# Kernel tuning notes

Hardware: AMD Instinct MI355X
Metric: run time of the kernel (lower is better)

Reference implementation:

```python
import jax, jax.numpy as jnp
import numpy as np

N_NODES, N_EDGES, D, N_RELS = 50000, 600000, 128, 460


def setup_inputs() -> dict:
    key = jax.random.key(0)
    ks = jax.random.split(key, 8)
    h = jax.random.normal(ks[0], (N_NODES, D), dtype=jnp.float32)
    emb_rel = jax.random.normal(ks[1], (N_RELS, D), dtype=jnp.float32)
    attn_fc_w = jax.random.normal(ks[2], (D, 3 * D), dtype=jnp.float32) * 0.05   # Linear(3D->D), weight [out,in]
    attn_fc2_w = jax.random.normal(ks[3], (1, D), dtype=jnp.float32) * 0.05     # Linear(D->1)
    loop_weight = jax.random.normal(ks[4], (D, D), dtype=jnp.float32) * 0.05
    edge_src = jax.random.randint(ks[5], (N_EDGES,), 0, N_NODES)
    edge_dst = jax.random.randint(ks[6], (N_EDGES,), 0, N_NODES)
    edge_type = jax.random.randint(ks[7], (N_EDGES,), 0, N_RELS)
    return {"h": h, "emb_rel": emb_rel, "attn_fc_w": attn_fc_w,
            "attn_fc2_w": attn_fc2_w, "loop_weight": loop_weight,
            "edge_src": edge_src, "edge_dst": edge_dst, "edge_type": edge_type}


def reference(h, emb_rel, attn_fc_w, attn_fc2_w, loop_weight, edge_src, edge_dst, edge_type):
    n = h.shape[0]
    # --- per-edge gather ---
    hs = h[edge_src]            # [E, D] src features (mailbox 'e_h')
    ht = h[edge_dst]            # [E, D]
    rel = emb_rel[edge_type]    # [E, D]
    # --- concat-MLP attention: leaky_relu(fc2(fc1([hs|ht|rel]))) ---
    z2 = jnp.concatenate([hs, ht, rel], axis=1)          # [E, 3D]
    a = z2 @ attn_fc_w.T                                  # [E, D]
    e = jax.nn.leaky_relu(a @ attn_fc2_w.T)               # [E, 1], slope 0.01 (torch default)
    # --- per-destination segment softmax ---
    m = jax.ops.segment_max(e, edge_dst, num_segments=n)  # [N, 1]
    m = jnp.where(jnp.isfinite(m), m, jnp.float32(0.0))   # empty nodes -> -inf; neutralize
    ex = jnp.exp(e - m[edge_dst])                         # [E, 1]
    den = jax.ops.segment_sum(ex, edge_dst, num_segments=n)
    alpha = ex / den[edge_dst]                            # [E, 1]
    # --- weighted scatter-sum of src features ---
    node_repr = jax.ops.segment_sum(alpha * hs, edge_dst, num_segments=n)  # [N, D]
    # --- self-loop ---
    node_repr = node_repr + h @ loop_weight
    return node_repr
```

## Files before the change

kernel.cpp:

```cpp
#include <hip/hip_runtime.h>

#define N_NODES 50000
#define N_EDGES 600000
#define D 128
#define N_RELS 460
#define CAP_LOG 6

typedef unsigned short u16;
typedef __attribute__((ext_vector_type(8))) short bf16x8;
typedef __attribute__((ext_vector_type(4))) float f32x4;

enum : int {
    OFF_W      = 0,
    OFF_S1     = 384,
    OFF_S2     = 50384,
    OFF_S3     = 100384,
    OFF_COUNTS = 100864,
    OFF_CSR    = 900864,
    OFF_HB     = 4100864,
};

#define NODE_WAVES   12500
#define REL_WAVES    115
#define SCORE_BLOCKS 3154
#define GEMM_BLOCKS  782
#define ZERO_BLOCKS  196
#define FILL_BLOCKS  293
#define WT_STRIDE    136

__device__ __forceinline__ u16 f2bf(float f) {
    unsigned u = __float_as_uint(f);
    unsigned r = u + 0x7FFFu + ((u >> 16) & 1u);
    return (u16)(r >> 16);
}
__device__ __forceinline__ float blo(unsigned u) { return __uint_as_float(u << 16); }
__device__ __forceinline__ float bhi(unsigned u) { return __uint_as_float(u & 0xFFFF0000u); }

__global__ __launch_bounds__(256) void k_prep(
        const float* __restrict__ fc1, const float* __restrict__ fc2,
        const float* __restrict__ W, const float* __restrict__ h,
        float* __restrict__ w, int* __restrict__ counts,
        u16* __restrict__ hb, float* __restrict__ out) {
    __shared__ u16 Ws[D * WT_STRIDE];
    int t = threadIdx.x;
    if (blockIdx.x < GEMM_BLOCKS) {
        for (int i = t; i < (D * D) / 4; i += 256) {
            float4 v = ((const float4*)W)[i];
            int k  = i >> 5;
            int n0 = (i & 31) * 4;
            Ws[(n0 + 0) * WT_STRIDE + k] = f2bf(v.x);
            Ws[(n0 + 1) * WT_STRIDE + k] = f2bf(v.y);
            Ws[(n0 + 2) * WT_STRIDE + k] = f2bf(v.z);
            Ws[(n0 + 3) * WT_STRIDE + k] = f2bf(v.w);
        }
        __syncthreads();

        int wave = t >> 6, lane = t & 63;
        int quad = lane >> 4, m16 = lane & 15;
        int nbase = blockIdx.x * 64 + wave * 16;

        f32x4 acc[8];
        #pragma unroll
        for (int cg = 0; cg < 8; ++cg) acc[cg] = (f32x4){0.f, 0.f, 0.f, 0.f};

        int arow = nbase + m16;
        if (arow >= N_NODES) arow = N_NODES - 1;
        const float* aptr = h + (size_t)arow * D + quad * 8;
        u16* hbp = hb + (size_t)arow * D + quad * 8;

        #pragma unroll
        for (int k0 = 0; k0 < D; k0 += 32) {
            float4 a0 = *(const float4*)(aptr + k0);
            float4 a1 = *(const float4*)(aptr + k0 + 4);
            bf16x8 a;
            a[0] = (short)f2bf(a0.x); a[1] = (short)f2bf(a0.y);
            a[2] = (short)f2bf(a0.z); a[3] = (short)f2bf(a0.w);
            a[4] = (short)f2bf(a1.x); a[5] = (short)f2bf(a1.y);
            a[6] = (short)f2bf(a1.z); a[7] = (short)f2bf(a1.w);
            *(bf16x8*)(hbp + k0) = a;
            #pragma unroll
            for (int cg = 0; cg < 8; ++cg) {
                bf16x8 bb = *(const bf16x8*)(&Ws[(cg * 16 + m16) * WT_STRIDE + k0 + quad * 8]);
                acc[cg] = __builtin_amdgcn_mfma_f32_16x16x32_bf16(a, bb, acc[cg], 0, 0, 0);
            }
        }
        #pragma unroll
        for (int reg = 0; reg < 4; ++reg) {
            int row = nbase + quad * 4 + reg;
            if (row < N_NODES) {
                #pragma unroll
                for (int cg = 0; cg < 8; ++cg)
                    out[(size_t)row * D + cg * 16 + m16] = acc[cg][reg];
            }
        }
    } else if (blockIdx.x < GEMM_BLOCKS + ZERO_BLOCKS) {
        int i4 = (blockIdx.x - GEMM_BLOCKS) * 256 + t;
        #pragma unroll
        for (int rep = 0; rep < 4; ++rep) {
            int idx = i4 * 4 + rep;
            if (idx * 4 < N_NODES * 16)
                ((int4*)counts)[idx] = make_int4(0, 0, 0, 0);
        }
    } else {
        for (int j = t; j < 3 * D; j += 256) {
            float acc = 0.f;
            for (int k = 0; k < D; ++k) acc += fc2[k] * fc1[k * 3 * D + j];
            w[j] = acc;
        }
    }
}

__global__ __launch_bounds__(256) void k_fused(
        const int* __restrict__ src, const int* __restrict__ dst,
        const int* __restrict__ typ, int* __restrict__ counts,
        unsigned* __restrict__ csr,
        const u16* __restrict__ hb, const float* __restrict__ emb_rel,
        const float* __restrict__ w,
        float* __restrict__ s1, float* __restrict__ s2, float* __restrict__ s3) {
    if (blockIdx.x < FILL_BLOCKS) {
        int i = blockIdx.x * blockDim.x + threadIdx.x;
        if (i >= N_EDGES / 8) return;
        int4 da = ((const int4*)dst)[2 * i],     db = ((const int4*)dst)[2 * i + 1];
        int4 sa = ((const int4*)src)[2 * i],     sb = ((const int4*)src)[2 * i + 1];
        int4 ta = ((const int4*)typ)[2 * i],     tb = ((const int4*)typ)[2 * i + 1];
        int l0 = atomicAdd(&counts[da.x << 4], 1);
        int l1 = atomicAdd(&counts[da.y << 4], 1);
        int l2 = atomicAdd(&counts[da.z << 4], 1);
        int l3 = atomicAdd(&counts[da.w << 4], 1);
        int l4 = atomicAdd(&counts[db.x << 4], 1);
        int l5 = atomicAdd(&counts[db.y << 4], 1);
        int l6 = atomicAdd(&counts[db.z << 4], 1);
        int l7 = atomicAdd(&counts[db.w << 4], 1);
        csr[(da.x << CAP_LOG) + l0] = (unsigned)sa.x | ((unsigned)ta.x << 16);
        csr[(da.y << CAP_LOG) + l1] = (unsigned)sa.y | ((unsigned)ta.y << 16);
        csr[(da.z << CAP_LOG) + l2] = (unsigned)sa.z | ((unsigned)ta.z << 16);
        csr[(da.w << CAP_LOG) + l3] = (unsigned)sa.w | ((unsigned)ta.w << 16);
        csr[(db.x << CAP_LOG) + l4] = (unsigned)sb.x | ((unsigned)tb.x << 16);
        csr[(db.y << CAP_LOG) + l5] = (unsigned)sb.y | ((unsigned)tb.y << 16);
        csr[(db.z << CAP_LOG) + l6] = (unsigned)sb.z | ((unsigned)tb.z << 16);
        csr[(db.w << CAP_LOG) + l7] = (unsigned)sb.w | ((unsigned)tb.w << 16);
    } else {
        int wv = ((blockIdx.x - FILL_BLOCKS) * blockDim.x + threadIdx.x) >> 6;
        int l  = threadIdx.x & 63;
        int sub = l >> 4;
        int q   = l & 15;
        if (wv < NODE_WAVES) {
            int r = wv * 4 + sub;
            uint4 pk = ((const uint4*)hb)[(size_t)r * 16 + q];
            float4 w10 = *(const float4*)(w + q * 8);
            float4 w11 = *(const float4*)(w + q * 8 + 4);
            float4 w20 = *(const float4*)(w + D + q * 8);
            float4 w21 = *(const float4*)(w + D + q * 8 + 4);
            float a1 = blo(pk.x) * w10.x + bhi(pk.x) * w10.y
                     + blo(pk.y) * w10.z + bhi(pk.y) * w10.w
                     + blo(pk.z) * w11.x + bhi(pk.z) * w11.y
                     + blo(pk.w) * w11.z + bhi(pk.w) * w11.w;
            float a2 = blo(pk.x) * w20.x + bhi(pk.x) * w20.y
                     + blo(pk.y) * w20.z + bhi(pk.y) * w20.w
                     + blo(pk.z) * w21.x + bhi(pk.z) * w21.y
                     + blo(pk.w) * w21.z + bhi(pk.w) * w21.w;
            #pragma unroll
            for (int o = 8; o; o >>= 1) { a1 += __shfl_xor(a1, o, 16); a2 += __shfl_xor(a2, o, 16); }
            if (q == 0) { s1[r] = a1; s2[r] = a2; }
        } else if (wv < NODE_WAVES + REL_WAVES) {
            int r = (wv - NODE_WAVES) * 4 + sub;
            const float* rp = emb_rel + (size_t)r * D + q * 8;
            float4 r0 = *(const float4*)rp;
            float4 r1 = *(const float4*)(rp + 4);
            float4 w30 = *(const float4*)(w + 2 * D + q * 8);
            float4 w31 = *(const float4*)(w + 2 * D + q * 8 + 4);
            float a3 = r0.x * w30.x + r0.y * w30.y + r0.z * w30.z + r0.w * w30.w
                     + r1.x * w31.x + r1.y * w31.y + r1.z * w31.z + r1.w * w31.w;
            #pragma unroll
            for (int o = 8; o; o >>= 1) a3 += __shfl_xor(a3, o, 16);
            if (q == 0) s3[r] = a3;
        }
    }
}

#define ROWACC(uu, cc)                                                         \
    accA.x += (cc) * blo((uu).x);  accA.y += (cc) * bhi((uu).x);               \
    accA.z += (cc) * blo((uu).y);  accA.w += (cc) * bhi((uu).y);               \
    accB.x += (cc) * blo((uu).z);  accB.y += (cc) * bhi((uu).z);               \
    accB.z += (cc) * blo((uu).w);  accB.w += (cc) * bhi((uu).w);

__global__ void k_gather(const u16* __restrict__ hb, const int* __restrict__ counts,
                         const unsigned* __restrict__ csr,
                         const float* __restrict__ s1, const float* __restrict__ s2,
                         const float* __restrict__ s3, float* __restrict__ out) {
    int n  = (blockIdx.x * blockDim.x + threadIdx.x) >> 4;
    int gl = threadIdx.x & 15;
    if (n >= N_NODES) return;
    int deg = counts[n << 4];
    if (deg == 0) return;
    int beg = n << CAP_LOG;
    int end = beg + deg;

    float s2n = s2[n];
    float den = 0.f;
    f32x4 accA = {0.f, 0.f, 0.f, 0.f}, accB = {0.f, 0.f, 0.f, 0.f};

    for (int cb = beg; cb < end; cb += 16) {
        int i = cb + gl;
        int msrc = 0; float mex = 0.f;
        if (i < end) {
            unsigned p = csr[i];
            msrc = (int)(p & 0xFFFFu);
            float x = s1[msrc] + s2n + s3[p >> 16];
            float lv = (x > 0.f) ? x : 0.01f * x;
            mex = __expf(lv);
        }
        den += mex;
        int cnt = min(16, end - cb);
        int j = 0;
        for (; j + 7 < cnt; j += 8) {
            int aa[8]; float cc[8]; uint4 uu[8];
            #pragma unroll
            for (int u = 0; u < 8; ++u) {
                aa[u] = __shfl(msrc, j + u, 16);
                cc[u] = __shfl(mex,  j + u, 16);
            }
            #pragma unroll
            for (int u = 0; u < 8; ++u)
                uu[u] = ((const uint4*)(hb + (size_t)aa[u] * D))[gl];
            #pragma unroll
            for (int u = 0; u < 8; ++u) { ROWACC(uu[u], cc[u]); }
        }
        for (; j + 3 < cnt; j += 4) {
            int aa[4]; float cc[4]; uint4 uu[4];
            #pragma unroll
            for (int u = 0; u < 4; ++u) {
                aa[u] = __shfl(msrc, j + u, 16);
                cc[u] = __shfl(mex,  j + u, 16);
            }
            #pragma unroll
            for (int u = 0; u < 4; ++u)
                uu[u] = ((const uint4*)(hb + (size_t)aa[u] * D))[gl];
            #pragma unroll
            for (int u = 0; u < 4; ++u) { ROWACC(uu[u], cc[u]); }
        }
        for (; j < cnt; ++j) {
            int   a0 = __shfl(msrc, j, 16);
            float c0 = __shfl(mex, j, 16);
            uint4 u0 = ((const uint4*)(hb + (size_t)a0 * D))[gl];
            ROWACC(u0, c0);
        }
    }
    #pragma unroll
    for (int o = 8; o; o >>= 1) den += __shfl_xor(den, o, 16);
    float inv = 1.f / den;

    f32x4* op = (f32x4*)(out + (size_t)n * D + gl * 8);
    f32x4 o0 = __builtin_nontemporal_load(op);
    f32x4 o1 = __builtin_nontemporal_load(op + 1);
    o0 += accA * inv;
    o1 += accB * inv;
    __builtin_nontemporal_store(o0, op);
    __builtin_nontemporal_store(o1, op + 1);
}

extern "C" void kernel_launch(void* const* d_in, const int* in_sizes, int n_in,
                              void* d_out, int out_size, void* d_ws, size_t ws_size,
                              hipStream_t stream) {
    const float* h       = (const float*)d_in[0];
    const float* emb_rel = (const float*)d_in[1];
    const float* fc1     = (const float*)d_in[2];
    const float* fc2     = (const float*)d_in[3];
    const float* loopw   = (const float*)d_in[4];
    const int*   esrc    = (const int*)d_in[5];
    const int*   edst    = (const int*)d_in[6];
    const int*   etyp    = (const int*)d_in[7];
    float* out = (float*)d_out;
    float* ws  = (float*)d_ws;

    float*    w       = ws + OFF_W;
    float*    s1      = ws + OFF_S1;
    float*    s2      = ws + OFF_S2;
    float*    s3      = ws + OFF_S3;
    int*      counts  = (int*)(ws + OFF_COUNTS);
    unsigned* csr     = (unsigned*)(ws + OFF_CSR);
    u16*      hb      = (u16*)(ws + OFF_HB);

    k_prep<<<GEMM_BLOCKS + ZERO_BLOCKS + 1, 256, 0, stream>>>(
        fc1, fc2, loopw, h, w, counts, hb, out);

    k_fused<<<FILL_BLOCKS + SCORE_BLOCKS, 256, 0, stream>>>(
        esrc, edst, etyp, counts, csr, hb, emb_rel, w, s1, s2, s3);

    k_gather<<<(N_NODES * 16 + 255) / 256, 256, 0, stream>>>(
        hb, counts, csr, s1, s2, s3, out);
}
```

Before: 170.1 us.

## Fuse self-loop GEMM into gather kernel and move bf16 conversion into score pass

```diff
diff --git a/kernel.cpp b/kernel.cpp
--- a/kernel.cpp
+++ b/kernel.cpp
@@ -23,9 +23,9 @@
 #define NODE_WAVES   12500
 #define REL_WAVES    115
 #define SCORE_BLOCKS 3154
-#define GEMM_BLOCKS  782
 #define ZERO_BLOCKS  196
 #define FILL_BLOCKS  293
+#define GG_BLOCKS    782
 #define WT_STRIDE    136
 
 __device__ __forceinline__ u16 f2bf(float f) {
@@ -36,77 +36,23 @@
 __device__ __forceinline__ float blo(unsigned u) { return __uint_as_float(u << 16); }
 __device__ __forceinline__ float bhi(unsigned u) { return __uint_as_float(u & 0xFFFF0000u); }
 
-__global__ __launch_bounds__(256) void k_prep(
-        const float* __restrict__ fc1, const float* __restrict__ fc2,
-        const float* __restrict__ W, const float* __restrict__ h,
-        float* __restrict__ w, int* __restrict__ counts,
-        u16* __restrict__ hb, float* __restrict__ out) {
-    __shared__ u16 Ws[D * WT_STRIDE];
-    int t = threadIdx.x;
-    if (blockIdx.x < GEMM_BLOCKS) {
-        for (int i = t; i < (D * D) / 4; i += 256) {
-            float4 v = ((const float4*)W)[i];
-            int k  = i >> 5;
-            int n0 = (i & 31) * 4;
-            Ws[(n0 + 0) * WT_STRIDE + k] = f2bf(v.x);
-            Ws[(n0 + 1) * WT_STRIDE + k] = f2bf(v.y);
-            Ws[(n0 + 2) * WT_STRIDE + k] = f2bf(v.z);
-            Ws[(n0 + 3) * WT_STRIDE + k] = f2bf(v.w);
-        }
-        __syncthreads();
-
-        int wave = t >> 6, lane = t & 63;
-        int quad = lane >> 4, m16 = lane & 15;
-        int nbase = blockIdx.x * 64 + wave * 16;
-
-        f32x4 acc[8];
-        #pragma unroll
-        for (int cg = 0; cg < 8; ++cg) acc[cg] = (f32x4){0.f, 0.f, 0.f, 0.f};
-
-        int arow = nbase + m16;
-        if (arow >= N_NODES) arow = N_NODES - 1;
-        const float* aptr = h + (size_t)arow * D + quad * 8;
-        u16* hbp = hb + (size_t)arow * D + quad * 8;
-
-        #pragma unroll
-        for (int k0 = 0; k0 < D; k0 += 32) {
-            float4 a0 = *(const float4*)(aptr + k0);
-            float4 a1 = *(const float4*)(aptr + k0 + 4);
-            bf16x8 a;
-            a[0] = (short)f2bf(a0.x); a[1] = (short)f2bf(a0.y);
-            a[2] = (short)f2bf(a0.z); a[3] = (short)f2bf(a0.w);
-            a[4] = (short)f2bf(a1.x); a[5] = (short)f2bf(a1.y);
-            a[6] = (short)f2bf(a1.z); a[7] = (short)f2bf(a1.w);
-            *(bf16x8*)(hbp + k0) = a;
-            #pragma unroll
-            for (int cg = 0; cg < 8; ++cg) {
-                bf16x8 bb = *(const bf16x8*)(&Ws[(cg * 16 + m16) * WT_STRIDE + k0 + quad * 8]);
-                acc[cg] = __builtin_amdgcn_mfma_f32_16x16x32_bf16(a, bb, acc[cg], 0, 0, 0);
-            }
-        }
-        #pragma unroll
-        for (int reg = 0; reg < 4; ++reg) {
-            int row = nbase + quad * 4 + reg;
-            if (row < N_NODES) {
-                #pragma unroll
-                for (int cg = 0; cg < 8; ++cg)
-                    out[(size_t)row * D + cg * 16 + m16] = acc[cg][reg];
-            }
-        }
-    } else if (blockIdx.x < GEMM_BLOCKS + ZERO_BLOCKS) {
-        int i4 = (blockIdx.x - GEMM_BLOCKS) * 256 + t;
+__global__ void k_prep(const float* __restrict__ fc1, const float* __restrict__ fc2,
+                       float* __restrict__ w, int* __restrict__ counts) {
+    int b = blockIdx.x, t = threadIdx.x;
+    if (b == 0) {
+        for (int j = t; j < 3 * D; j += 256) {
+            float acc = 0.f;
+            for (int k = 0; k < D; ++k) acc += fc2[k] * fc1[k * 3 * D + j];
+            w[j] = acc;
+        }
+    } else {
+        int i4 = (b - 1) * 256 + t;
         #pragma unroll
         for (int rep = 0; rep < 4; ++rep) {
             int idx = i4 * 4 + rep;
             if (idx * 4 < N_NODES * 16)
                 ((int4*)counts)[idx] = make_int4(0, 0, 0, 0);
         }
-    } else {
-        for (int j = t; j < 3 * D; j += 256) {
-            float acc = 0.f;
-            for (int k = 0; k < D; ++k) acc += fc2[k] * fc1[k * 3 * D + j];
-            w[j] = acc;
-        }
     }
 }
 
@@ -114,9 +60,10 @@
         const int* __restrict__ src, const int* __restrict__ dst,
         const int* __restrict__ typ, int* __restrict__ counts,
         unsigned* __restrict__ csr,
-        const u16* __restrict__ hb, const float* __restrict__ emb_rel,
+        const float* __restrict__ h, const float* __restrict__ emb_rel,
         const float* __restrict__ w,
-        float* __restrict__ s1, float* __restrict__ s2, float* __restrict__ s3) {
+        float* __restrict__ s1, float* __restrict__ s2, float* __restrict__ s3,
+        u16* __restrict__ hb) {
     if (blockIdx.x < FILL_BLOCKS) {
         int i = blockIdx.x * blockDim.x + threadIdx.x;
         if (i >= N_EDGES / 8) return;
@@ -146,19 +93,23 @@
         int q   = l & 15;
         if (wv < NODE_WAVES) {
             int r = wv * 4 + sub;
-            uint4 pk = ((const uint4*)hb)[(size_t)r * 16 + q];
+            const float* hp = h + (size_t)r * D + q * 8;
+            float4 h0 = *(const float4*)hp;
+            float4 h1 = *(const float4*)(hp + 4);
+            uint4 pk;
+            pk.x = (unsigned)f2bf(h0.x) | ((unsigned)f2bf(h0.y) << 16);
+            pk.y = (unsigned)f2bf(h0.z) | ((unsigned)f2bf(h0.w) << 16);
+            pk.z = (unsigned)f2bf(h1.x) | ((unsigned)f2bf(h1.y) << 16);
+            pk.w = (unsigned)f2bf(h1.z) | ((unsigned)f2bf(h1.w) << 16);
+            ((uint4*)hb)[(size_t)r * 16 + q] = pk;
             float4 w10 = *(const float4*)(w + q * 8);
             float4 w11 = *(const float4*)(w + q * 8 + 4);
             float4 w20 = *(const float4*)(w + D + q * 8);
             float4 w21 = *(const float4*)(w + D + q * 8 + 4);
-            float a1 = blo(pk.x) * w10.x + bhi(pk.x) * w10.y
-                     + blo(pk.y) * w10.z + bhi(pk.y) * w10.w
-                     + blo(pk.z) * w11.x + bhi(pk.z) * w11.y
-                     + blo(pk.w) * w11.z + bhi(pk.w) * w11.w;
-            float a2 = blo(pk.x) * w20.x + bhi(pk.x) * w20.y
-                     + blo(pk.y) * w20.z + bhi(pk.y) * w20.w
-                     + blo(pk.z) * w21.x + bhi(pk.z) * w21.y
-                     + blo(pk.w) * w21.z + bhi(pk.w) * w21.w;
+            float a1 = h0.x * w10.x + h0.y * w10.y + h0.z * w10.z + h0.w * w10.w
+                     + h1.x * w11.x + h1.y * w11.y + h1.z * w11.z + h1.w * w11.w;
+            float a2 = h0.x * w20.x + h0.y * w20.y + h0.z * w20.z + h0.w * w20.w
+                     + h1.x * w21.x + h1.y * w21.y + h1.z * w21.z + h1.w * w21.w;
             #pragma unroll
             for (int o = 8; o; o >>= 1) { a1 += __shfl_xor(a1, o, 16); a2 += __shfl_xor(a2, o, 16); }
             if (q == 0) { s1[r] = a1; s2[r] = a2; }
@@ -184,79 +135,132 @@
     accB.x += (cc) * blo((uu).z);  accB.y += (cc) * bhi((uu).z);               \
     accB.z += (cc) * blo((uu).w);  accB.w += (cc) * bhi((uu).w);
 
-__global__ void k_gather(const u16* __restrict__ hb, const int* __restrict__ counts,
-                         const unsigned* __restrict__ csr,
-                         const float* __restrict__ s1, const float* __restrict__ s2,
-                         const float* __restrict__ s3, float* __restrict__ out) {
-    int n  = (blockIdx.x * blockDim.x + threadIdx.x) >> 4;
-    int gl = threadIdx.x & 15;
-    if (n >= N_NODES) return;
-    int deg = counts[n << 4];
-    if (deg == 0) return;
-    int beg = n << CAP_LOG;
-    int end = beg + deg;
-
-    float s2n = s2[n];
-    float den = 0.f;
-    f32x4 accA = {0.f, 0.f, 0.f, 0.f}, accB = {0.f, 0.f, 0.f, 0.f};
-
-    for (int cb = beg; cb < end; cb += 16) {
-        int i = cb + gl;
-        int msrc = 0; float mex = 0.f;
-        if (i < end) {
-            unsigned p = csr[i];
-            msrc = (int)(p & 0xFFFFu);
-            float x = s1[msrc] + s2n + s3[p >> 16];
-            float lv = (x > 0.f) ? x : 0.01f * x;
-            mex = __expf(lv);
-        }
-        den += mex;
-        int cnt = min(16, end - cb);
-        int j = 0;
-        for (; j + 7 < cnt; j += 8) {
-            int aa[8]; float cc[8]; uint4 uu[8];
-            #pragma unroll
-            for (int u = 0; u < 8; ++u) {
-                aa[u] = __shfl(msrc, j + u, 16);
-                cc[u] = __shfl(mex,  j + u, 16);
-            }
-            #pragma unroll
-            for (int u = 0; u < 8; ++u)
-                uu[u] = ((const uint4*)(hb + (size_t)aa[u] * D))[gl];
-            #pragma unroll
-            for (int u = 0; u < 8; ++u) { ROWACC(uu[u], cc[u]); }
-        }
-        for (; j + 3 < cnt; j += 4) {
-            int aa[4]; float cc[4]; uint4 uu[4];
-            #pragma unroll
-            for (int u = 0; u < 4; ++u) {
-                aa[u] = __shfl(msrc, j + u, 16);
-                cc[u] = __shfl(mex,  j + u, 16);
-            }
-            #pragma unroll
-            for (int u = 0; u < 4; ++u)
-                uu[u] = ((const uint4*)(hb + (size_t)aa[u] * D))[gl];
-            #pragma unroll
-            for (int u = 0; u < 4; ++u) { ROWACC(uu[u], cc[u]); }
-        }
-        for (; j < cnt; ++j) {
-            int   a0 = __shfl(msrc, j, 16);
-            float c0 = __shfl(mex, j, 16);
-            uint4 u0 = ((const uint4*)(hb + (size_t)a0 * D))[gl];
-            ROWACC(u0, c0);
-        }
-    }
+__global__ __launch_bounds__(256) void k_gather_gemm(
+        const float* __restrict__ W, const u16* __restrict__ hb,
+        const int* __restrict__ counts, const unsigned* __restrict__ csr,
+        const float* __restrict__ s1, const float* __restrict__ s2,
+        const float* __restrict__ s3, float* __restrict__ out) {
+    __shared__ u16 Ws[D * WT_STRIDE];
+    float* LDSf = (float*)Ws;
+    int t = threadIdx.x;
+
+    for (int i = t; i < (D * D) / 4; i += 256) {
+        float4 v = ((const float4*)W)[i];
+        int k  = i >> 5;
+        int n0 = (i & 31) * 4;
+        Ws[(n0 + 0) * WT_STRIDE + k] = f2bf(v.x);
+        Ws[(n0 + 1) * WT_STRIDE + k] = f2bf(v.y);
+        Ws[(n0 + 2) * WT_STRIDE + k] = f2bf(v.z);
+        Ws[(n0 + 3) * WT_STRIDE + k] = f2bf(v.w);
+    }
+    __syncthreads();
+
+    int wave = t >> 6, lane = t & 63;
+    int quad = lane >> 4, m16 = lane & 15;
+    int nbase = blockIdx.x * 64 + wave * 16;
+
+    f32x4 acc[8];
     #pragma unroll
-    for (int o = 8; o; o >>= 1) den += __shfl_xor(den, o, 16);
-    float inv = 1.f / den;
-
-    f32x4* op = (f32x4*)(out + (size_t)n * D + gl * 8);
-    f32x4 o0 = __builtin_nontemporal_load(op);
-    f32x4 o1 = __builtin_nontemporal_load(op + 1);
-    o0 += accA * inv;
-    o1 += accB * inv;
-    __builtin_nontemporal_store(o0, op);
-    __builtin_nontemporal_store(o1, op + 1);
+    for (int cg = 0; cg < 8; ++cg) acc[cg] = (f32x4){0.f, 0.f, 0.f, 0.f};
+
+    int arow = nbase + m16;
+    if (arow >= N_NODES) arow = N_NODES - 1;
+    const u16* aptr = hb + (size_t)arow * D + quad * 8;
+
+    #pragma unroll
+    for (int k0 = 0; k0 < D; k0 += 32) {
+        bf16x8 a = *(const bf16x8*)(aptr + k0);
+        #pragma unroll
+        for (int cg = 0; cg < 8; ++cg) {
+            bf16x8 bb = *(const bf16x8*)(&Ws[(cg * 16 + m16) * WT_STRIDE + k0 + quad * 8]);
+            acc[cg] = __builtin_amdgcn_mfma_f32_16x16x32_bf16(a, bb, acc[cg], 0, 0, 0);
+        }
+    }
+    __syncthreads();
+
+    #pragma unroll
+    for (int reg = 0; reg < 4; ++reg) {
+        int lrow = wave * 16 + quad * 4 + reg;
+        #pragma unroll
+        for (int cg = 0; cg < 8; ++cg)
+            LDSf[lrow * D + cg * 16 + m16] = acc[cg][reg];
+    }
+    __syncthreads();
+
+    int g  = t >> 4;
+    int gl = t & 15;
+    for (int k = 0; k < 4; ++k) {
+        int ln = g * 4 + k;
+        int n  = blockIdx.x * 64 + ln;
+        if (n >= N_NODES) continue;
+        int deg = counts[n << 4];
+        float* op = out + (size_t)n * D + gl * 8;
+        f32x4 base0 = *(f32x4*)(&LDSf[ln * D + gl * 8]);
+        f32x4 base1 = *(f32x4*)(&LDSf[ln * D + gl * 8 + 4]);
+        if (deg == 0) {
+            *(f32x4*)op = base0;
+            *(f32x4*)(op + 4) = base1;
+            continue;
+        }
+        int beg = n << CAP_LOG;
+        int end = beg + deg;
+        float s2n = s2[n];
+        float den = 0.f;
+        f32x4 accA = {0.f, 0.f, 0.f, 0.f}, accB = {0.f, 0.f, 0.f, 0.f};
+
+        for (int cb = beg; cb < end; cb += 16) {
+            int i = cb + gl;
+            int msrc = 0; float mex = 0.f;
+            if (i < end) {
+                unsigned p = csr[i];
+                msrc = (int)(p & 0xFFFFu);
+                float x = s1[msrc] + s2n + s3[p >> 16];
+                float lv = (x > 0.f) ? x : 0.01f * x;
+                mex = __expf(lv);
+            }
+            den += mex;
+            int cnt = min(16, end - cb);
+            int j = 0;
+            for (; j + 7 < cnt; j += 8) {
+                int aa[8]; float cc[8]; uint4 uu[8];
+                #pragma unroll
+                for (int u = 0; u < 8; ++u) {
+                    aa[u] = __shfl(msrc, j + u, 16);
+                    cc[u] = __shfl(mex,  j + u, 16);
+                }
+                #pragma unroll
+                for (int u = 0; u < 8; ++u)
+                    uu[u] = ((const uint4*)(hb + (size_t)aa[u] * D))[gl];
+                #pragma unroll
+                for (int u = 0; u < 8; ++u) { ROWACC(uu[u], cc[u]); }
+            }
+            for (; j + 3 < cnt; j += 4) {
+                int aa[4]; float cc[4]; uint4 uu[4];
+                #pragma unroll
+                for (int u = 0; u < 4; ++u) {
+                    aa[u] = __shfl(msrc, j + u, 16);
+                    cc[u] = __shfl(mex,  j + u, 16);
+                }
+                #pragma unroll
+                for (int u = 0; u < 4; ++u)
+                    uu[u] = ((const uint4*)(hb + (size_t)aa[u] * D))[gl];
+                #pragma unroll
+                for (int u = 0; u < 4; ++u) { ROWACC(uu[u], cc[u]); }
+            }
+            for (; j < cnt; ++j) {
+                int   a0 = __shfl(msrc, j, 16);
+                float c0 = __shfl(mex, j, 16);
+                uint4 u0 = ((const uint4*)(hb + (size_t)a0 * D))[gl];
+                ROWACC(u0, c0);
+            }
+        }
+        #pragma unroll
+        for (int o = 8; o; o >>= 1) den += __shfl_xor(den, o, 16);
+        float inv = 1.f / den;
+
+        *(f32x4*)op       = base0 + accA * inv;
+        *(f32x4*)(op + 4) = base1 + accB * inv;
+    }
 }
 
 extern "C" void kernel_launch(void* const* d_in, const int* in_sizes, int n_in,
@@ -281,12 +285,11 @@
     unsigned* csr     = (unsigned*)(ws + OFF_CSR);
     u16*      hb      = (u16*)(ws + OFF_HB);
 
-    k_prep<<<GEMM_BLOCKS + ZERO_BLOCKS + 1, 256, 0, stream>>>(
-        fc1, fc2, loopw, h, w, counts, hb, out);
+    k_prep<<<1 + ZERO_BLOCKS, 256, 0, stream>>>(fc1, fc2, w, counts);
 
     k_fused<<<FILL_BLOCKS + SCORE_BLOCKS, 256, 0, stream>>>(
-        esrc, edst, etyp, counts, csr, hb, emb_rel, w, s1, s2, s3);
-
-    k_gather<<<(N_NODES * 16 + 255) / 256, 256, 0, stream>>>(
-        hb, counts, csr, s1, s2, s3, out);
-}
+        esrc, edst, etyp, counts, csr, h, emb_rel, w, s1, s2, s3, hb);
+
+    k_gather_gemm<<<GG_BLOCKS, 256, 0, stream>>>(
+        loopw, hb, counts, csr, s1, s2, s3, out);
+}
```

Measured after the change: 192.3 us. +13.0%, slower.
